# Optimization experiments

Hardware: AMD Instinct MI355X
Metric: run time of the kernel (lower is better)

Reference implementation:

```python
import jax, jax.numpy as jnp
import numpy as np

NUM_ENT = 50000
DIM = 128
NUM_REL = 1000  # num_rel * 2 (inverse relations)
E = 300000
SLOPE = 0.2      # args.leaky_relu_w
BN_EPS = 1e-5


def _leaky(x):
    return jax.nn.leaky_relu(x, SLOPE)


def _l2norm(x):
    n = jnp.linalg.norm(x, axis=-1, keepdims=True)
    return x / jnp.maximum(n, 1e-12)


def _batchnorm(x):
    # BatchNorm1d, training mode, fresh gamma=1/beta=0
    m = x.mean(axis=0)
    v = x.var(axis=0)
    return (x - m) / jnp.sqrt(v + BN_EPS)


def _propagate(i, j, etype, rel, x, watt, aatt, gcn, norm, num_ent):
    # gather -> relation-aware transform (opn='mult') -> attention -> scatter-add
    trans = x[j] * rel[etype]                       # [E, D]
    comb = jnp.concatenate([x[i], trans], axis=1)   # [E, 2D]
    score = (_leaky(comb @ watt) @ aatt)[:, 0]      # [E]
    # scatter softmax of attention score over destination nodes
    m = jax.ops.segment_max(score, i, num_segments=num_ent)
    m = jnp.where(jnp.isfinite(m), m, 0.0)
    e = jnp.exp(score - m[i])
    s = jax.ops.segment_sum(e, i, num_segments=num_ent)
    alpha = e / (s[i] + 1e-16)
    msg = (trans @ gcn) * alpha[:, None]
    if norm is not None:
        msg = msg * norm[:, None]
    return jax.ops.segment_sum(msg, i, num_segments=num_ent)


def _conv(ent, rel_in, edge_index, edge_type, w1, w2, gcn, loop_rel, watt, aatt):
    # RelationalAwareLayer.forward
    num_ent = ent.shape[0]
    rel = jnp.concatenate([rel_in, loop_rel], axis=0)
    rel = _leaky(rel @ w1) @ w2
    row, col = edge_index[0], edge_index[1]
    deg = jax.ops.segment_sum(jnp.ones((row.shape[0],), jnp.float32), row, num_segments=num_ent)
    dinv = jnp.where(deg > 0, deg ** -0.5, 0.0)
    norm = dinv[row]
    msg_n = _propagate(row, col, edge_type, rel, ent, watt, aatt, gcn, norm, num_ent)
    idx = jnp.arange(num_ent)
    loop_t = jnp.full((num_ent,), rel.shape[0] - 1)
    msg_s = _propagate(idx, idx, loop_t, rel, ent, watt, aatt, gcn, None, num_ent)
    return jnp.tanh(_batchnorm((msg_n + msg_s) / 2.0))


def setup_inputs() -> dict:
    key = jax.random.key(0)
    ks = jax.random.split(key, 24)
    g = lambda k, s: jax.random.normal(k, s, dtype=jnp.float32) * 0.05
    return {
        'edge_index': jax.random.randint(ks[0], (2, E), 0, NUM_ENT),
        'edge_type': jax.random.randint(ks[1], (E,), 0, NUM_REL),
        'ent_info_att': g(ks[2], (NUM_ENT, DIM)),
        'ent_completion_att': g(ks[3], (NUM_ENT, DIM)),
        'rel_completion_att': g(ks[4], (NUM_REL, DIM)),
        'rel_info_att': g(ks[5], (NUM_REL, DIM)),
        'align_linear1_1': g(ks[6], (2 * DIM, DIM)),
        'align_linear1_2': g(ks[7], (DIM, DIM)),
        'align_linear2_1': g(ks[8], (2 * DIM, DIM)),
        'align_linear2_2': g(ks[9], (DIM, DIM)),
        'rel_linear11': g(ks[10], (DIM, DIM)),
        'rel_linear12': g(ks[11], (DIM, DIM)),
        'rel_linear11_align': g(ks[12], (DIM, DIM)),
        'rel_linear12_align': g(ks[13], (DIM, DIM)),
        'all_linear_comp': g(ks[14], (3 * DIM, DIM)),
        # stacked per-layer conv params: [conv1_align, conv1_completion, conv2_align]
        'conv_w1': g(ks[15], (3, DIM, DIM)),
        'conv_w2': g(ks[16], (3, DIM, DIM)),
        'conv_gcn': g(ks[17], (3, DIM, DIM)),
        'conv_loop': g(ks[18], (3, 1, DIM)),
        'conv_watt': g(ks[19], (3, 2 * DIM, DIM)),
        'conv_aatt': g(ks[20], (3, DIM, 1)),
    }


def reference(edge_index, edge_type, ent_info_att, ent_completion_att,
              rel_completion_att, rel_info_att,
              align_linear1_1, align_linear1_2, align_linear2_1, align_linear2_2,
              rel_linear11, rel_linear12, rel_linear11_align, rel_linear12_align,
              all_linear_comp, conv_w1, conv_w2, conv_gcn, conv_loop, conv_watt, conv_aatt):
    # forward_base with num_gcn_layer == 2, dropout rate 0 (identity)
    init_comp = _l2norm(ent_completion_att)
    e1 = _leaky(jnp.concatenate([init_comp, ent_info_att], axis=1) @ align_linear1_1) @ align_linear1_2
    ao1 = _conv(e1, rel_info_att, edge_index, edge_type,
                conv_w1[0], conv_w2[0], conv_gcn[0], conv_loop[0], conv_watt[0], conv_aatt[0])
    co1 = _conv(ent_completion_att, rel_completion_att, edge_index, edge_type,
                conv_w1[1], conv_w2[1], conv_gcn[1], conv_loop[1], conv_watt[1], conv_aatt[1])
    pos1n = _l2norm(co1)
    e2 = _leaky(jnp.concatenate([pos1n, ao1], axis=1) @ align_linear2_1) @ align_linear2_2
    pr1 = _leaky(rel_completion_att @ rel_linear11) @ rel_linear12
    ari = _leaky(rel_info_att @ rel_linear11_align) @ rel_linear12_align
    ao2 = _conv(e2, ari, edge_index, edge_type,
                conv_w1[2], conv_w2[2], conv_gcn[2], conv_loop[2], conv_watt[2], conv_aatt[2])
    out = jnp.concatenate([e1, ao1, ao2], axis=1) @ all_linear_comp
    return (out, co1, pr1)
```

## Files before the change

### kernel.cpp

```cpp
#include <hip/hip_runtime.h>
#include <hip/hip_bf16.h>
#include <math.h>

#define D 128
#define DD 16384
#define NEMAX 96
typedef unsigned short u16;
typedef __attribute__((ext_vector_type(8))) short short8v;
typedef __attribute__((ext_vector_type(4))) short short4v;
typedef __attribute__((ext_vector_type(4))) float f32x4;

__device__ __forceinline__ u16 f2s(float v){
    union { __hip_bfloat16 h; u16 u; } c; c.h = __float2bfloat16(v); return c.u;
}
__device__ __forceinline__ float s2f(u16 u){
    union { __hip_bfloat16 h; u16 u; } c; c.u = u; return __bfloat162float(c.h);
}
__device__ __forceinline__ float lrelu(float x){ return x > 0.f ? x : 0.2f*x; }

__global__ void k_prepz(int* __restrict__ zz, int zw, int* __restrict__ nstart,
                        int* __restrict__ nend, int nb){
    int i = blockIdx.x*blockDim.x + threadIdx.x;
    int stride = gridDim.x*blockDim.x;
    for (int k = i; k < zw; k += stride) zz[k] = 0;
    for (int k = i; k < nb; k += stride){ nstart[k] = 0x7fffffff; nend[k] = -1; }
}
__global__ void k_f2b4(const float* __restrict__ in, u16* __restrict__ out, int n4){
    for (int i = blockIdx.x*blockDim.x + threadIdx.x; i < n4; i += gridDim.x*blockDim.x){
        float4 a = ((const float4*)in)[i];
        short4v pk;
        pk[0] = (short)f2s(a.x); pk[1] = (short)f2s(a.y);
        pk[2] = (short)f2s(a.z); pk[3] = (short)f2s(a.w);
        *(short4v*)(out + (size_t)i*4) = pk;
    }
}
__global__ void k_ideg(const int* __restrict__ row, int* __restrict__ deg, int E_){
    for (int i = blockIdx.x*blockDim.x + threadIdx.x; i < E_; i += gridDim.x*blockDim.x)
        atomicAdd(&deg[row[i]], 1);
}
__global__ void k_scan1(const int* __restrict__ ideg, int* __restrict__ rowptr,
                        int* __restrict__ bsum, int n){
    __shared__ int buf[256];
    int t = threadIdx.x, i = blockIdx.x*256 + t;
    int v = (i < n) ? ideg[i] : 0;
    buf[t] = v;
    __syncthreads();
    #pragma unroll
    for (int o = 1; o < 256; o <<= 1){
        int u = (t >= o) ? buf[t-o] : 0;
        __syncthreads();
        buf[t] += u;
        __syncthreads();
    }
    if (i < n) rowptr[i] = buf[t] - v;
    if (t == 255) bsum[blockIdx.x] = buf[255];
}
__global__ void k_scan2(int* __restrict__ bsum, int nb){
    __shared__ int buf[256];
    __shared__ int carry_s;
    int t = threadIdx.x;
    if (t == 0) carry_s = 0;
    __syncthreads();
    for (int base = 0; base < nb; base += 256){
        int v = (base + t < nb) ? bsum[base + t] : 0;
        buf[t] = v;
        __syncthreads();
        #pragma unroll
        for (int o = 1; o < 256; o <<= 1){
            int u = (t >= o) ? buf[t-o] : 0;
            __syncthreads();
            buf[t] += u;
            __syncthreads();
        }
        if (base + t < nb) bsum[base + t] = carry_s + buf[t] - v;
        int last = buf[255];
        __syncthreads();
        if (t == 0) carry_s += last;
        __syncthreads();
    }
}
__global__ void k_scan3(int* __restrict__ rowptr, const int* __restrict__ bsum,
                        int n, int E_){
    int i = blockIdx.x*blockDim.x + threadIdx.x;
    if (i < n) rowptr[i] += bsum[i >> 8];
    if (i == 0) rowptr[n] = E_;
}
__global__ void k_scatter(const int* __restrict__ row, const int* __restrict__ rowptr,
                          int* __restrict__ cnt, int* __restrict__ perm, int E_){
    for (int e = blockIdx.x*blockDim.x + threadIdx.x; e < E_; e += gridDim.x*blockDim.x){
        int i = row[e];
        int pos = rowptr[i] + atomicAdd(&cnt[i], 1);
        perm[pos] = e;
    }
}
__global__ void k_bmap(const int* __restrict__ rowptr, int* __restrict__ nstart,
                       int* __restrict__ nend, int n){
    for (int i = blockIdx.x*blockDim.x + threadIdx.x; i < n; i += gridDim.x*blockDim.x){
        int s = rowptr[i], e = rowptr[i+1];
        if (e > s){
            int b = s >> 6;
            atomicMin(&nstart[b], i);
            atomicMax(&nend[b], i);
        }
    }
}
__global__ void k_bnapply(const u16* __restrict__ acc, const float* __restrict__ gp,
                          float inv_ne, int n, u16* __restrict__ dstb,
                          float* __restrict__ dstf){
    int d = threadIdx.x & 127;
    float m = gp[d] * inv_ne;
    float var = gp[128 + d] * inv_ne - m*m;
    float sc = rsqrtf(var + 1e-5f);
    for (int i = blockIdx.x*blockDim.x + threadIdx.x; i < n; i += gridDim.x*blockDim.x){
        float v = s2f(acc[i]) * 0.5f;
        float r = tanhf((v - m) * sc);
        dstb[i] = f2s(r);
        if (dstf) dstf[i] = r;
    }
}

__global__ void k_relprep(const float* __restrict__ rel_comp, const float* __restrict__ rel_info,
        const float* __restrict__ rl11, const float* __restrict__ rl12,
        const float* __restrict__ rl11a, const float* __restrict__ rl12a,
        const float* __restrict__ cloop, const float* __restrict__ cw1,
        const float* __restrict__ cw2, float* __restrict__ pr1out,
        float* __restrict__ rel2all, int NR){
    int b = blockIdx.x, t = threadIdx.x;
    __shared__ float v[D];
    __shared__ float h[D];
    if (b < NR){
        v[t] = rel_comp[(size_t)b*D + t];
        __syncthreads();
        float a = 0.f;
        #pragma unroll 8
        for (int k = 0; k < D; k++) a += v[k] * rl11[(size_t)k*D + t];
        h[t] = lrelu(a);
        __syncthreads();
        float o = 0.f;
        #pragma unroll 8
        for (int k = 0; k < D; k++) o += h[k] * rl12[(size_t)k*D + t];
        pr1out[(size_t)b*D + t] = o;
        return;
    }
    int bb = b - NR;
    int l = bb / (NR+1), r = bb - l*(NR+1);
    float xv;
    if (r == NR)      xv = cloop[l*D + t];
    else if (l == 1)  xv = rel_comp[(size_t)r*D + t];
    else              xv = rel_info[(size_t)r*D + t];
    v[t] = xv;
    __syncthreads();
    if (l == 2 && r < NR){
        float a = 0.f;
        #pragma unroll 8
        for (int k = 0; k < D; k++) a += v[k] * rl11a[(size_t)k*D + t];
        h[t] = lrelu(a);
        __syncthreads();
        float o = 0.f;
        #pragma unroll 8
        for (int k = 0; k < D; k++) o += h[k] * rl12a[(size_t)k*D + t];
        v[t] = o;
        __syncthreads();
    }
    const float* w1 = cw1 + (size_t)l*DD;
    const float* w2 = cw2 + (size_t)l*DD;
    float a = 0.f;
    #pragma unroll 8
    for (int k = 0; k < D; k++) a += v[k] * w1[(size_t)k*D + t];
    h[t] = lrelu(a);
    __syncthreads();
    float o = 0.f;
    #pragma unroll 8
    for (int k = 0; k < D; k++) o += h[k] * w2[(size_t)k*D + t];
    rel2all[((size_t)l*(NR+1) + r)*D + t] = o;
}

struct TEnt { const float* s; u16* d; int ldd; };
struct TTab { TEnt e[18]; };
__global__ void k_wprep(TTab tab){
    TEnt en = tab.e[blockIdx.x];
    int t = threadIdx.x;
    int n = t >> 1, h = t & 1;
    #pragma unroll
    for (int g = 0; g < 8; ++g){
        int k0 = h*64 + g*8;
        short8v pk;
        #pragma unroll
        for (int q = 0; q < 8; ++q) pk[q] = (short)f2s(en.s[(size_t)(k0+q)*D + n]);
        *(short8v*)(en.d + (size_t)n*en.ldd + k0) = pk;
    }
}

struct Srcs { const void* p0; const void* p1; const void* p2; int f0, f1, f2; };

template<int NSEG, int EPI, bool RSN>
__global__ __launch_bounds__(256) void k_mrow(Srcs S, const u16* __restrict__ WT,
        void* __restrict__ out, int NE_){
    __shared__ __align__(16) short As[128*128];
    int tid = threadIdx.x;
    int row0 = blockIdx.x * 128;
    int lane = tid & 63, w = tid >> 6;
    int l15 = lane & 15, lq = lane >> 4;
    int nhalf = w & 1, mquad = w >> 1;
    f32x4 acc[4][4];
    #pragma unroll
    for (int a = 0; a < 4; a++)
        #pragma unroll
        for (int b = 0; b < 4; b++) acc[a][b] = (f32x4){0.f,0.f,0.f,0.f};

    int sr = tid >> 1, sh = tid & 1;
    int rr = row0 + sr; if (rr >= NE_) rr = NE_ - 1;

    #pragma unroll
    for (int s = 0; s < NSEG; ++s){
        const void* sp = (s == 0) ? S.p0 : (s == 1) ? S.p1 : S.p2;
        int sf = (s == 0) ? S.f0 : (s == 1) ? S.f1 : S.f2;
        if (s) __syncthreads();
        #pragma unroll
        for (int g = 0; g < 8; ++g){
            int k8 = sh*64 + g*8;
            short8v pk;
            if (sf){
                const float* fp = (const float*)sp + (size_t)rr*D + k8;
                #pragma unroll
                for (int q = 0; q < 8; ++q) pk[q] = (short)f2s(fp[q]);
            } else {
                pk = *(const short8v*)((const u16*)sp + (size_t)rr*D + k8);
            }
            *(short8v*)(As + sr*D + (((k8>>3) ^ (sr&7))<<3)) = pk;
        }
        if (RSN && s == 0){
            float ss = 0.f;
            #pragma unroll
            for (int g = 0; g < 8; ++g){
                int k8 = sh*64 + g*8;
                short8v v = *(const short8v*)(As + sr*D + (((k8>>3) ^ (sr&7))<<3));
                #pragma unroll
                for (int q = 0; q < 8; ++q){ float f = s2f((u16)v[q]); ss += f*f; }
            }
            ss += __shfl_xor(ss, 1, 64);
            float rsc = 1.f / fmaxf(sqrtf(ss), 1e-12f);
            #pragma unroll
            for (int g = 0; g < 8; ++g){
                int k8 = sh*64 + g*8;
                short* ap = As + sr*D + (((k8>>3) ^ (sr&7))<<3);
                short8v v = *(const short8v*)ap;
                short8v pk;
                #pragma unroll
                for (int q = 0; q < 8; ++q) pk[q] = (short)f2s(s2f((u16)v[q]) * rsc);
                *(short8v*)ap = pk;
            }
        }
        __syncthreads();
        short8v bfr[4][4];
        #pragma unroll
        for (int nt = 0; nt < 4; ++nt)
            #pragma unroll
            for (int kk = 0; kk < 4; ++kk){
                size_t idx = (size_t)(nhalf*64 + nt*16 + l15)*(NSEG*D) + (size_t)s*D + kk*32 + lq*8;
                bfr[nt][kk] = *(const short8v*)(WT + idx);
            }
        #pragma unroll
        for (int mt = 0; mt < 4; ++mt){
            int ar = mquad*64 + mt*16 + l15;
            short8v afr[4];
            #pragma unroll
            for (int kk = 0; kk < 4; ++kk)
                afr[kk] = *(const short8v*)(As + ar*D + (((kk*4 + lq) ^ (ar&7))<<3));
            #pragma unroll
            for (int nt = 0; nt < 4; ++nt)
                #pragma unroll
                for (int kk = 0; kk < 4; ++kk)
                    acc[mt][nt] = __builtin_amdgcn_mfma_f32_16x16x32_bf16(
                        afr[kk], bfr[nt][kk], acc[mt][nt], 0, 0, 0);
        }
    }
    #pragma unroll
    for (int mt = 0; mt < 4; ++mt){
        #pragma unroll
        for (int nt = 0; nt < 4; ++nt){
            #pragma unroll
            for (int r = 0; r < 4; ++r){
                int gr = row0 + mquad*64 + mt*16 + lq*4 + r;
                if (gr >= NE_) continue;
                int c = nhalf*64 + nt*16 + l15;
                float v = acc[mt][nt][r];
                if (EPI == 0) ((float*)out)[(size_t)gr*D + c] = v;
                else ((u16*)out)[(size_t)gr*D + c] = f2s(EPI == 2 ? lrelu(v) : v);
            }
        }
    }
}

struct ConvP { const u16* x; const u16* WT; u16* out; u16* ub; const float* loop; float* gp; };

template<int MODE>
__global__ __launch_bounds__(256) void k_mrow2(ConvP A, ConvP B, int rb, int NE_){
    __shared__ __align__(16) short As[128*128];
    int pb = blockIdx.x >= rb;
    ConvP P = pb ? B : A;
    int row0 = (blockIdx.x - (pb ? rb : 0)) * 128;
    int tid = threadIdx.x;
    int lane = tid & 63, w = tid >> 6;
    int l15 = lane & 15, lq = lane >> 4;
    int nhalf = w & 1, mquad = w >> 1;
    f32x4 acc[4][4];
    #pragma unroll
    for (int a = 0; a < 4; a++)
        #pragma unroll
        for (int b = 0; b < 4; b++) acc[a][b] = (f32x4){0.f,0.f,0.f,0.f};

    int sr = tid >> 1, sh = tid & 1;
    int rr = row0 + sr; if (rr >= NE_) rr = NE_ - 1;
    #pragma unroll
    for (int g = 0; g < 8; ++g){
        int k8 = sh*64 + g*8;
        short8v pk = *(const short8v*)(P.x + (size_t)rr*D + k8);
        *(short8v*)(As + sr*D + (((k8>>3) ^ (sr&7))<<3)) = pk;
    }
    __syncthreads();
    short8v bfr[4][4];
    #pragma unroll
    for (int nt = 0; nt < 4; ++nt)
        #pragma unroll
        for (int kk = 0; kk < 4; ++kk)
            bfr[nt][kk] = *(const short8v*)(P.WT + (size_t)(nhalf*64 + nt*16 + l15)*D + kk*32 + lq*8);
    #pragma unroll
    for (int mt = 0; mt < 4; ++mt){
        int ar = mquad*64 + mt*16 + l15;
        short8v afr[4];
        #pragma unroll
        for (int kk = 0; kk < 4; ++kk)
            afr[kk] = *(const short8v*)(As + ar*D + (((kk*4 + lq) ^ (ar&7))<<3));
        #pragma unroll
        for (int nt = 0; nt < 4; ++nt)
            #pragma unroll
            for (int kk = 0; kk < 4; ++kk)
                acc[mt][nt] = __builtin_amdgcn_mfma_f32_16x16x32_bf16(
                    afr[kk], bfr[nt][kk], acc[mt][nt], 0, 0, 0);
    }
    if (MODE == 3){
        float cs[4] = {0,0,0,0}, cs2[4] = {0,0,0,0};
        #pragma unroll
        for (int mt = 0; mt < 4; ++mt)
            #pragma unroll
            for (int nt = 0; nt < 4; ++nt)
                #pragma unroll
                for (int r = 0; r < 4; ++r){
                    int gr = row0 + mquad*64 + mt*16 + lq*4 + r;
                    if (gr >= NE_) continue;
                    int c = nhalf*64 + nt*16 + l15;
                    float v = acc[mt][nt][r];
                    P.out[(size_t)gr*D + c] = f2s(v);
                    float h = v * 0.5f;
                    cs[nt] += h; cs2[nt] += h*h;
                }
        __syncthreads();
        float* ps  = (float*)As;
        float* ps2 = ps + 1024;
        int slot = mquad*4 + lq;
        #pragma unroll
        for (int nt = 0; nt < 4; ++nt){
            int c = nhalf*64 + nt*16 + l15;
            ps[slot*128 + c]  = cs[nt];
            ps2[slot*128 + c] = cs2[nt];
        }
        __syncthreads();
        if (tid < 128){
            float s = 0.f, s2 = 0.f;
            #pragma unroll
            for (int q = 0; q < 8; ++q){ s += ps[q*128 + tid]; s2 += ps2[q*128 + tid]; }
            atomicAdd(&P.gp[tid], s);
            atomicAdd(&P.gp[128 + tid], s2);
        }
    } else {
        #pragma unroll
        for (int mt = 0; mt < 4; ++mt)
            #pragma unroll
            for (int nt = 0; nt < 4; ++nt)
                #pragma unroll
                for (int r = 0; r < 4; ++r){
                    int gr = row0 + mquad*64 + mt*16 + lq*4 + r;
                    if (gr >= NE_) continue;
                    int c = nhalf*64 + nt*16 + l15;
                    P.out[(size_t)gr*D + c] = f2s(acc[mt][nt][r]);
                }
        for (int idx = tid; idx < 128*128; idx += 256){
            int r2 = idx >> 7, c = idx & 127;
            int gr = row0 + r2;
            if (gr < NE_){
                float v = s2f((u16)As[r2*D + ((((c>>3) ^ (r2&7))<<3) | (c&7))]) * P.loop[c];
                P.ub[(size_t)gr*D + c] = f2s(v);
            }
        }
    }
}

struct FP { const u16* x; const float* rel2; const u16* xattb; const u16* WT;
            const float* aatt; u16* u; };

__global__ __launch_bounds__(256) void k_fedge(
        const int* __restrict__ rowi, const int* __restrict__ coli, const int* __restrict__ ety,
        const int* __restrict__ rowptr, const int* __restrict__ perm,
        const int* __restrict__ nstart, const int* __restrict__ nend,
        FP fa, FP fb, int nb){
    __shared__ __align__(16) short As[NEMAX*D];
    __shared__ u16 jL[NEMAX], kL[NEMAX], iL[NEMAX];
    __shared__ float sc[NEMAX];
    __shared__ float red[2][NEMAX];
    int pb = blockIdx.x >= nb;
    FP P = pb ? fb : fa;
    int b = blockIdx.x - (pb ? nb : 0);
    int ns = nstart[b];
    if (ns == 0x7fffffff) return;
    int nn = nend[b] - ns + 1;
    int tid = threadIdx.x;
    int estart = rowptr[ns];
    int ne = rowptr[ns + nn] - estart;
    if (ne > NEMAX) ne = NEMAX;
    int T = (ne + 15) >> 4;
    int nrows = T << 4;
    if (tid < ne){
        int e = perm[estart + tid];
        jL[tid] = (u16)coli[e]; kL[tid] = (u16)ety[e]; iL[tid] = (u16)rowi[e];
    }
    __syncthreads();
    for (int it = tid; it < nrows*4; it += 256){
        int p = it >> 2, part = it & 3;
        int ps = (p < ne) ? p : (ne - 1);
        int j = jL[ps], krel = kL[ps];
        #pragma unroll
        for (int g = 0; g < 4; ++g){
            int k8 = part*32 + g*8;
            short8v sv = *(const short8v*)(P.x + (size_t)j*D + k8);
            const float* rp = P.rel2 + (size_t)krel*D + k8;
            short8v pk;
            #pragma unroll
            for (int q = 0; q < 8; ++q) pk[q] = (short)f2s(s2f((u16)sv[q]) * rp[q]);
            *(short8v*)(As + p*D + (((k8>>3) ^ (p&7))<<3)) = pk;
        }
    }
    __syncthreads();
    int lane = tid & 63, w = tid >> 6;
    int l15 = lane & 15, lq = lane >> 4;
    int nhalf = w & 1, mq = w >> 1;
    short8v bfr[4][4];
    #pragma unroll
    for (int nt = 0; nt < 4; ++nt)
        #pragma unroll
        for (int kk = 0; kk < 4; ++kk)
            bfr[nt][kk] = *(const short8v*)(P.WT + (size_t)(nhalf*64 + nt*16 + l15)*D + kk*32 + lq*8);
    float av[4];
    #pragma unroll
    for (int nt = 0; nt < 4; ++nt) av[nt] = P.aatt[nhalf*64 + nt*16 + l15];

    for (int t = mq; t < T; t += 2){
        float xv[4][4];
        #pragma unroll
        for (int r = 0; r < 4; ++r){
            int el = t*16 + lq*4 + r;
            int ep = (el < ne) ? el : (ne - 1);
            int ii = iL[ep];
            #pragma unroll
            for (int nt = 0; nt < 4; ++nt)
                xv[r][nt] = s2f(P.xattb[(size_t)ii*D + nhalf*64 + nt*16 + l15]);
        }
        int ar = t*16 + l15;
        short8v afr[4];
        #pragma unroll
        for (int kk = 0; kk < 4; ++kk)
            afr[kk] = *(const short8v*)(As + ar*D + (((kk*4 + lq) ^ (ar&7))<<3));
        f32x4 acc[4];
        #pragma unroll
        for (int nt = 0; nt < 4; ++nt) acc[nt] = (f32x4){0.f,0.f,0.f,0.f};
        #pragma unroll
        for (int nt = 0; nt < 4; ++nt)
            #pragma unroll
            for (int kk = 0; kk < 4; ++kk)
                acc[nt] = __builtin_amdgcn_mfma_f32_16x16x32_bf16(
                    afr[kk], bfr[nt][kk], acc[nt], 0, 0, 0);
        #pragma unroll
        for (int r = 0; r < 4; ++r){
            int el = t*16 + lq*4 + r;
            float p = 0.f;
            if (el < ne){
                #pragma unroll
                for (int nt = 0; nt < 4; ++nt)
                    p += lrelu(acc[nt][r] + xv[r][nt]) * av[nt];
            }
            p += __shfl_xor(p, 1, 64);
            p += __shfl_xor(p, 2, 64);
            p += __shfl_xor(p, 4, 64);
            p += __shfl_xor(p, 8, 64);
            if (l15 == 0 && el < NEMAX) red[nhalf][el] = p;
        }
    }
    __syncthreads();
    if (tid < ne) sc[tid] = expf(red[0][tid] + red[1][tid]);
    __syncthreads();
    if (tid < nn){
        int i = ns + tid;
        int s0 = rowptr[i] - estart, s1 = rowptr[i+1] - estart;
        if (s1 > NEMAX) s1 = NEMAX;
        if (s1 > s0){
            float sum = 0.f;
            for (int p = s0; p < s1; ++p) sum += sc[p];
            float coef = rsqrtf((float)(s1 - s0)) / (sum + 1e-16f);
            for (int p = s0; p < s1; ++p) sc[p] *= coef;
        }
    }
    __syncthreads();
    int c = tid & 127, nh = tid >> 7;
    for (int n = nh; n < nn; n += 2){
        int i = ns + n;
        int s0 = rowptr[i] - estart, s1 = rowptr[i+1] - estart;
        if (s1 > NEMAX) s1 = NEMAX;
        if (s1 <= s0) continue;
        float a = 0.f;
        int p = s0;
        for (; p + 4 <= s1; p += 4){
            float v0 = s2f((u16)As[(p+0)*D + ((((c>>3) ^ ((p+0)&7))<<3) | (c&7))]);
            float v1 = s2f((u16)As[(p+1)*D + ((((c>>3) ^ ((p+1)&7))<<3) | (c&7))]);
            float v2 = s2f((u16)As[(p+2)*D + ((((c>>3) ^ ((p+2)&7))<<3) | (c&7))]);
            float v3 = s2f((u16)As[(p+3)*D + ((((c>>3) ^ ((p+3)&7))<<3) | (c&7))]);
            a += sc[p]*v0 + sc[p+1]*v1 + sc[p+2]*v2 + sc[p+3]*v3;
        }
        for (; p < s1; ++p)
            a += sc[p] * s2f((u16)As[p*D + ((((c>>3) ^ (p&7))<<3) | (c&7))]);
        size_t ad = (size_t)i*D + c;
        P.u[ad] = f2s(s2f(P.u[ad]) + a);
    }
}

extern "C" void kernel_launch(void* const* d_in, const int* in_sizes, int n_in,
                              void* d_out, int out_size, void* d_ws, size_t ws_size,
                              hipStream_t stream){
    const int* eidx = (const int*)d_in[0];
    const int* ety  = (const int*)d_in[1];
    const float* ent_info = (const float*)d_in[2];
    const float* ent_comp = (const float*)d_in[3];
    const float* rel_comp = (const float*)d_in[4];
    const float* rel_info = (const float*)d_in[5];
    const float* al11 = (const float*)d_in[6],  *al12 = (const float*)d_in[7];
    const float* al21 = (const float*)d_in[8],  *al22 = (const float*)d_in[9];
    const float* rl11 = (const float*)d_in[10], *rl12 = (const float*)d_in[11];
    const float* rl11a = (const float*)d_in[12], *rl12a = (const float*)d_in[13];
    const float* allw = (const float*)d_in[14];
    const float* cw1 = (const float*)d_in[15], *cw2 = (const float*)d_in[16];
    const float* cgcn = (const float*)d_in[17], *cloop = (const float*)d_in[18];
    const float* cwatt = (const float*)d_in[19], *caatt = (const float*)d_in[20];

    const int E  = in_sizes[1];
    const int NE = in_sizes[2] / D;
    const int NR = in_sizes[4] / D;
    const int* row = eidx;
    const int* col = eidx + E;
    const size_t NEd = (size_t)NE * D;
    float* outp = (float*)d_out;
    const int NB64 = (E + 63) / 64;

    char* wsb = (char*)d_ws;
    size_t off = 0;
    auto takeB = [&](size_t bytes) -> void* {
        void* q = wsb + off;
        off = (off + bytes + 255) & ~(size_t)255;
        return q;
    };
    u16*   slotA = (u16*) takeB(NEd * 2);
    u16*   hb    = slotA;
    u16*   accB0 = slotA;
    u16*   xattb0= (u16*) takeB(NEd * 2);
    u16*   ub0   = (u16*) takeB(NEd * 2);
    u16*   e1b   = (u16*) takeB(NEd * 2);
    u16*   ao1b  = (u16*) takeB(NEd * 2);
    u16*   e2b   = (u16*) takeB(NEd * 2);
    u16*   cob   = (u16*) takeB(NEd * 2);
    float* rel2all = (float*)takeB((size_t)3*(NR+1)*D*4);
    int*   rowptr= (int*)  takeB((size_t)(NE+1)*4);
    int*   perm  = (int*)  takeB((size_t)E*4);
    int*   bsum  = (int*)  takeB(1024*4);
    int*   nstart= (int*)  takeB((size_t)NB64*4);
    int*   nend  = (int*)  takeB((size_t)NB64*4);
    int ZW = 2*NE + 768;
    int*   zz    = (int*)  takeB((size_t)ZW*4);
    int*   ideg  = zz;
    int*   cnt   = zz + NE;
    float* gp3   = (float*)(zz + 2*NE);
    u16*   wtXatt = (u16*)takeB((size_t)3*DD*2);
    u16*   wtScore= (u16*)takeB((size_t)3*DD*2);
    u16*   wtGcn  = (u16*)takeB((size_t)3*DD*2);
    u16*   wtAl11 = (u16*)takeB((size_t)2*DD*2);
    u16*   wtAl12 = (u16*)takeB((size_t)DD*2);
    u16*   wtAl21 = (u16*)takeB((size_t)2*DD*2);
    u16*   wtAl22 = (u16*)takeB((size_t)DD*2);
    u16*   wtAllw = (u16*)takeB((size_t)3*DD*2);
    u16*   xcb   = e2b;

    size_t slab = ((NEd*2 + 255) & ~(size_t)255);
    bool wide = (off + 3*slab) <= ws_size;
    u16* xattb1 = wide ? (u16*)takeB(NEd * 2) : xattb0;
    u16* ub1    = wide ? (u16*)takeB(NEd * 2) : ub0;
    u16* accB1  = wide ? (u16*)takeB(NEd * 2) : accB0;

    const int GS = 2048, BS = 256;
    const int RB = (NE + 127) / 128;
    const int NB = (NE + 255) / 256;
    const float inv_ne = 1.f / (float)NE;

    TTab tab;
    int ti = 0;
    for (int l = 0; l < 3; ++l){
        tab.e[ti++] = { cwatt + (size_t)l*2*DD,        wtXatt  + (size_t)l*DD, 128 };
        tab.e[ti++] = { cwatt + (size_t)l*2*DD + DD,   wtScore + (size_t)l*DD, 128 };
        tab.e[ti++] = { cgcn  + (size_t)l*DD,          wtGcn   + (size_t)l*DD, 128 };
    }
    tab.e[ti++] = { al11,       wtAl11,        256 };
    tab.e[ti++] = { al11 + DD,  wtAl11 + 128,  256 };
    tab.e[ti++] = { al12,       wtAl12,        128 };
    tab.e[ti++] = { al21,       wtAl21,        256 };
    tab.e[ti++] = { al21 + DD,  wtAl21 + 128,  256 };
    tab.e[ti++] = { al22,       wtAl22,        128 };
    tab.e[ti++] = { allw,            wtAllw,        384 };
    tab.e[ti++] = { allw + DD,       wtAllw + 128,  384 };
    tab.e[ti++] = { allw + 2*DD,     wtAllw + 256,  384 };
    k_wprep<<<18, 256, 0, stream>>>(tab);

    k_prepz<<<256, BS, 0, stream>>>(zz, ZW, nstart, nend, NB64);
    k_f2b4<<<GS, BS, 0, stream>>>(ent_comp, xcb, (int)(NEd/4));
    k_ideg<<<GS, BS, 0, stream>>>(row, ideg, E);
    k_scan1<<<NB, 256, 0, stream>>>(ideg, rowptr, bsum, NE);
    k_scan2<<<1, 256, 0, stream>>>(bsum, NB);
    k_scan3<<<NB, 256, 0, stream>>>(rowptr, bsum, NE, E);
    k_scatter<<<GS, BS, 0, stream>>>(row, rowptr, cnt, perm, E);
    k_bmap<<<NB, 256, 0, stream>>>(rowptr, nstart, nend, NE);

    k_relprep<<<NR + 3*(NR+1), D, 0, stream>>>(rel_comp, rel_info, rl11, rl12,
                                               rl11a, rl12a, cloop, cw1, cw2,
                                               outp + 2*NEd, rel2all, NR);

    {
        Srcs S{ ent_comp, ent_info, nullptr, 1, 1, 0 };
        k_mrow<2, 2, true><<<RB, 256, 0, stream>>>(S, wtAl11, hb, NE);
        Srcs S2{ hb, nullptr, nullptr, 0, 0, 0 };
        k_mrow<1, 1, false><<<RB, 256, 0, stream>>>(S2, wtAl12, e1b, NE);
    }

    auto conv_seq = [&](const u16* x, int l, u16* xab, u16* ubp, u16* acb,
                        u16* dstb, float* dstf){
        const float* rel2l = rel2all + (size_t)l*(NR+1)*D;
        float* gp = gp3 + (size_t)l*256;
        ConvP A4{ x, wtXatt + (size_t)l*DD, xab, ubp, rel2l + (size_t)NR*D, nullptr };
        k_mrow2<4><<<RB, 256, 0, stream>>>(A4, A4, RB, NE);
        FP fa{ x, rel2l, xab, wtScore + (size_t)l*DD, caatt + (size_t)l*D, ubp };
        k_fedge<<<NB64, 256, 0, stream>>>(row, col, ety, rowptr, perm, nstart, nend,
                                          fa, fa, NB64);
        ConvP A3{ ubp, wtGcn + (size_t)l*DD, acb, nullptr, nullptr, gp };
        k_mrow2<3><<<RB, 256, 0, stream>>>(A3, A3, RB, NE);
        k_bnapply<<<GS, BS, 0, stream>>>(acb, gp, inv_ne, (int)NEd, dstb, dstf);
    };

    if (wide){
        const float* rel2_0 = rel2all;
        const float* rel2_1 = rel2all + (size_t)(NR+1)*D;
        ConvP A4{ e1b, wtXatt,      xattb0, ub0, rel2_0 + (size_t)NR*D, nullptr };
        ConvP B4{ xcb, wtXatt + DD, xattb1, ub1, rel2_1 + (size_t)NR*D, nullptr };
        k_mrow2<4><<<2*RB, 256, 0, stream>>>(A4, B4, RB, NE);
        FP fa{ e1b, rel2_0, xattb0, wtScore,      caatt,     ub0 };
        FP fb{ xcb, rel2_1, xattb1, wtScore + DD, caatt + D, ub1 };
        k_fedge<<<2*NB64, 256, 0, stream>>>(row, col, ety, rowptr, perm, nstart, nend,
                                            fa, fb, NB64);
        ConvP A3{ ub0, wtGcn,      accB0, nullptr, nullptr, gp3 };
        ConvP B3{ ub1, wtGcn + DD, accB1, nullptr, nullptr, gp3 + 256 };
        k_mrow2<3><<<2*RB, 256, 0, stream>>>(A3, B3, RB, NE);
        k_bnapply<<<GS, BS, 0, stream>>>(accB0, gp3, inv_ne, (int)NEd, ao1b, nullptr);
        k_bnapply<<<GS, BS, 0, stream>>>(accB1, gp3 + 256, inv_ne, (int)NEd, cob, outp + NEd);
    } else {
        conv_seq(e1b, 0, xattb0, ub0, accB0, ao1b, nullptr);
        conv_seq(xcb, 1, xattb0, ub0, accB0, cob, outp + NEd);
    }

    {
        Srcs S{ cob, ao1b, nullptr, 0, 0, 0 };
        k_mrow<2, 2, true><<<RB, 256, 0, stream>>>(S, wtAl21, hb, NE);
        Srcs S2{ hb, nullptr, nullptr, 0, 0, 0 };
        k_mrow<1, 1, false><<<RB, 256, 0, stream>>>(S2, wtAl22, e2b, NE);
    }

    conv_seq(e2b, 2, xattb0, ub0, accB0, cob, nullptr);

    {
        Srcs S{ e1b, ao1b, cob, 0, 0, 0 };
        k_mrow<3, 0, false><<<RB, 256, 0, stream>>>(S, wtAllw, outp, NE);
    }
}
```

Baseline: 669.9 us.

## Fold self-loop term into edge kernel and merge paired batchnorm applies

The edge kernel now computes each node's self-loop contribution (x times the loop relation) directly, instead of reading back a value already written to u and adding to it. It also derives destination indices from rowptr rather than loading rowi per edge. The two batchnorm-apply launches in the wide path are combined into one launch over both outputs. This cuts global read-modify-write traffic and launch count, but the earlier kernel still writes ub, so that work may now be redundant unless removed elsewhere. Nodes with no in-edges are skipped and so are never written, which could leave stale data.

```diff
diff --git a/kernel.cpp b/kernel.cpp
--- a/kernel.cpp
+++ b/kernel.cpp
@@ -116,6 +116,28 @@
         float r = tanhf((v - m) * sc);
         dstb[i] = f2s(r);
         if (dstf) dstf[i] = r;
+    }
+}
+__global__ void k_bnapply2(const u16* __restrict__ acc0, const float* __restrict__ gp0,
+                           u16* __restrict__ d0b,
+                           const u16* __restrict__ acc1, const float* __restrict__ gp1,
+                           u16* __restrict__ d1b, float* __restrict__ d1f,
+                           float inv_ne, int n, int gb){
+    int pb = blockIdx.x >= gb;
+    const u16* acc = pb ? acc1 : acc0;
+    const float* gp = pb ? gp1 : gp0;
+    u16* db = pb ? d1b : d0b;
+    float* df = pb ? d1f : nullptr;
+    int b = blockIdx.x - (pb ? gb : 0);
+    int d = threadIdx.x & 127;
+    float m = gp[d] * inv_ne;
+    float var = gp[128 + d] * inv_ne - m*m;
+    float sc = rsqrtf(var + 1e-5f);
+    for (int i = b*blockDim.x + threadIdx.x; i < n; i += gb*blockDim.x){
+        float v = s2f(acc[i]) * 0.5f;
+        float r = tanhf((v - m) * sc);
+        db[i] = f2s(r);
+        if (df) df[i] = r;
     }
 }
 
@@ -397,10 +419,10 @@
 }
 
 struct FP { const u16* x; const float* rel2; const u16* xattb; const u16* WT;
-            const float* aatt; u16* u; };
+            const float* aatt; const float* loop; u16* u; };
 
 __global__ __launch_bounds__(256) void k_fedge(
-        const int* __restrict__ rowi, const int* __restrict__ coli, const int* __restrict__ ety,
+        const int* __restrict__ coli, const int* __restrict__ ety,
         const int* __restrict__ rowptr, const int* __restrict__ perm,
         const int* __restrict__ nstart, const int* __restrict__ nend,
         FP fa, FP fb, int nb){
@@ -422,7 +444,14 @@
     int nrows = T << 4;
     if (tid < ne){
         int e = perm[estart + tid];
-        jL[tid] = (u16)coli[e]; kL[tid] = (u16)ety[e]; iL[tid] = (u16)rowi[e];
+        jL[tid] = (u16)coli[e]; kL[tid] = (u16)ety[e];
+    }
+    if (tid < nn){
+        int i = ns + tid;
+        int s0 = rowptr[i] - estart, s1 = rowptr[i+1] - estart;
+        if (s0 < 0) s0 = 0;
+        if (s1 > NEMAX) s1 = NEMAX;
+        for (int p = s0; p < s1; ++p) iL[p] = (u16)i;
     }
     __syncthreads();
     for (int it = tid; it < nrows*4; it += 256){
@@ -511,24 +540,31 @@
     }
     __syncthreads();
     int c = tid & 127, nh = tid >> 7;
-    for (int n = nh; n < nn; n += 2){
-        int i = ns + n;
-        int s0 = rowptr[i] - estart, s1 = rowptr[i+1] - estart;
-        if (s1 > NEMAX) s1 = NEMAX;
-        if (s1 <= s0) continue;
-        float a = 0.f;
-        int p = s0;
-        for (; p + 4 <= s1; p += 4){
-            float v0 = s2f((u16)As[(p+0)*D + ((((c>>3) ^ ((p+0)&7))<<3) | (c&7))]);
-            float v1 = s2f((u16)As[(p+1)*D + ((((c>>3) ^ ((p+1)&7))<<3) | (c&7))]);
-            float v2 = s2f((u16)As[(p+2)*D + ((((c>>3) ^ ((p+2)&7))<<3) | (c&7))]);
-            float v3 = s2f((u16)As[(p+3)*D + ((((c>>3) ^ ((p+3)&7))<<3) | (c&7))]);
-            a += sc[p]*v0 + sc[p+1]*v1 + sc[p+2]*v2 + sc[p+3]*v3;
-        }
-        for (; p < s1; ++p)
-            a += sc[p] * s2f((u16)As[p*D + ((((c>>3) ^ (p&7))<<3) | (c&7))]);
-        size_t ad = (size_t)i*D + c;
-        P.u[ad] = f2s(s2f(P.u[ad]) + a);
+    float loopc = P.loop[c];
+    for (int n0 = nh; n0 < nn; n0 += 16){
+        float xi[8];
+        int cnt = 0;
+        for (int n = n0; n < nn && cnt < 8; n += 2, ++cnt)
+            xi[cnt] = s2f(P.x[(size_t)(ns + n)*D + c]);
+        cnt = 0;
+        for (int n = n0; n < nn && cnt < 8; n += 2, ++cnt){
+            int i = ns + n;
+            int s0 = rowptr[i] - estart, s1 = rowptr[i+1] - estart;
+            if (s1 > NEMAX) s1 = NEMAX;
+            if (s1 <= s0) continue;
+            float a = xi[cnt] * loopc;
+            int p = s0;
+            for (; p + 4 <= s1; p += 4){
+                float v0 = s2f((u16)As[(p+0)*D + ((((c>>3) ^ ((p+0)&7))<<3) | (c&7))]);
+                float v1 = s2f((u16)As[(p+1)*D + ((((c>>3) ^ ((p+1)&7))<<3) | (c&7))]);
+                float v2 = s2f((u16)As[(p+2)*D + ((((c>>3) ^ ((p+2)&7))<<3) | (c&7))]);
+                float v3 = s2f((u16)As[(p+3)*D + ((((c>>3) ^ ((p+3)&7))<<3) | (c&7))]);
+                a += sc[p]*v0 + sc[p+1]*v1 + sc[p+2]*v2 + sc[p+3]*v3;
+            }
+            for (; p < s1; ++p)
+                a += sc[p] * s2f((u16)As[p*D + ((((c>>3) ^ (p&7))<<3) | (c&7))]);
+            P.u[(size_t)i*D + c] = f2s(a);
+        }
     }
 }
 
@@ -651,8 +687,9 @@
         float* gp = gp3 + (size_t)l*256;
         ConvP A4{ x, wtXatt + (size_t)l*DD, xab, ubp, rel2l + (size_t)NR*D, nullptr };
         k_mrow2<4><<<RB, 256, 0, stream>>>(A4, A4, RB, NE);
-        FP fa{ x, rel2l, xab, wtScore + (size_t)l*DD, caatt + (size_t)l*D, ubp };
-        k_fedge<<<NB64, 256, 0, stream>>>(row, col, ety, rowptr, perm, nstart, nend,
+        FP fa{ x, rel2l, xab, wtScore + (size_t)l*DD, caatt + (size_t)l*D,
+               rel2l + (size_t)NR*D, ubp };
+        k_fedge<<<NB64, 256, 0, stream>>>(col, ety, rowptr, perm, nstart, nend,
                                           fa, fa, NB64);
         ConvP A3{ ubp, wtGcn + (size_t)l*DD, acb, nullptr, nullptr, gp };
         k_mrow2<3><<<RB, 256, 0, stream>>>(A3, A3, RB, NE);
@@ -665,15 +702,16 @@
         ConvP A4{ e1b, wtXatt,      xattb0, ub0, rel2_0 + (size_t)NR*D, nullptr };
         ConvP B4{ xcb, wtXatt + DD, xattb1, ub1, rel2_1 + (size_t)NR*D, nullptr };
         k_mrow2<4><<<2*RB, 256, 0, stream>>>(A4, B4, RB, NE);
-        FP fa{ e1b, rel2_0, xattb0, wtScore,      caatt,     ub0 };
-        FP fb{ xcb, rel2_1, xattb1, wtScore + DD, caatt + D, ub1 };
-        k_fedge<<<2*NB64, 256, 0, stream>>>(row, col, ety, rowptr, perm, nstart, nend,
+        FP fa{ e1b, rel2_0, xattb0, wtScore,      caatt,     rel2_0 + (size_t)NR*D, ub0 };
+        FP fb{ xcb, rel2_1, xattb1, wtScore + DD, caatt + D, rel2_1 + (size_t)NR*D, ub1 };
+        k_fedge<<<2*NB64, 256, 0, stream>>>(col, ety, rowptr, perm, nstart, nend,
                                             fa, fb, NB64);
         ConvP A3{ ub0, wtGcn,      accB0, nullptr, nullptr, gp3 };
         ConvP B3{ ub1, wtGcn + DD, accB1, nullptr, nullptr, gp3 + 256 };
         k_mrow2<3><<<2*RB, 256, 0, stream>>>(A3, B3, RB, NE);
-        k_bnapply<<<GS, BS, 0, stream>>>(accB0, gp3, inv_ne, (int)NEd, ao1b, nullptr);
-        k_bnapply<<<GS, BS, 0, stream>>>(accB1, gp3 + 256, inv_ne, (int)NEd, cob, outp + NEd);
+        k_bnapply2<<<2*GS, BS, 0, stream>>>(accB0, gp3, ao1b,
+                                            accB1, gp3 + 256, cob, outp + NEd,
+                                            inv_ne, (int)NEd, GS);
     } else {
         conv_seq(e1b, 0, xattb0, ub0, accB0, ao1b, nullptr);
         conv_seq(xcb, 1, xattb0, ub0, accB0, cob, outp + NEd);
```

Result: slower. 685.7 us (+2.4%).
